# Optimization experiments

Measured on AMD Instinct MI355X. Metric: run time of the kernel, lower is better.

## Reference

```python
import jax, jax.numpy as jnp
import numpy as np

DIM = 512
WINDOW = 8
HEADS = 16
HEAD_DIM = DIM // HEADS
SIGMA = 0.39
B = 2048
N = WINDOW * WINDOW


def gaussian_kernel(window_size, sigma):
    """Row-normalised Gaussian attention mask K_sigma (M^2 x M^2)."""
    c = jnp.arange(window_size, dtype=jnp.float32)
    gy, gx = jnp.meshgrid(c, c, indexing='ij')
    pos = jnp.stack([gy.flatten(), gx.flatten()], -1)  # [M^2, 2]
    diff = pos[None, :, :] - pos[:, None, :]           # [M^2, M^2, 2]
    K = jnp.exp(-(diff ** 2).sum(-1) / (2.0 * sigma ** 2))
    return K / K.sum(-1, keepdims=True)


def setup_inputs() -> dict:
    key = jax.random.key(0)
    k1, k2, k3, k4, k5 = jax.random.split(key, 5)
    x = jax.random.normal(k1, (B, N, DIM), dtype=jnp.float32)
    # spectral_norm at inference is just a fixed scaling of the weight; we
    # model the (already-normalised) weights as plain dense params.
    w_qkv = jax.random.normal(k2, (DIM, 3 * DIM), dtype=jnp.float32) * (DIM ** -0.5)
    b_qkv = jax.random.normal(k3, (3 * DIM,), dtype=jnp.float32) * 0.02
    w_proj = jax.random.normal(k4, (DIM, DIM), dtype=jnp.float32) * (DIM ** -0.5)
    b_proj = jax.random.normal(k5, (DIM,), dtype=jnp.float32) * 0.02
    return {"x": x, "w_qkv": w_qkv, "b_qkv": b_qkv, "w_proj": w_proj, "b_proj": b_proj}


def reference(x, w_qkv, b_qkv, w_proj, b_proj):
    Bb, Nn, C = x.shape
    scale = HEAD_DIM ** -0.5
    qkv = (x @ w_qkv + b_qkv).reshape(Bb, Nn, 3, HEADS, HEAD_DIM)
    qkv = jnp.transpose(qkv, (2, 0, 3, 1, 4))  # [3, B, H, N, D]
    q, k, v = qkv[0], qkv[1], qkv[2]
    attn = jnp.einsum('bhnd,bhmd->bhnm', q, k) * scale  # [B, H, N, N]
    K_s = gaussian_kernel(WINDOW, SIGMA)                 # [N, N]
    attn = jax.nn.softmax(attn * K_s, axis=-1)
    out = jnp.einsum('bhnm,bhmd->bhnd', attn, v)         # [B, H, N, D]
    out = jnp.transpose(out, (0, 2, 1, 3)).reshape(Bb, Nn, C)
    return out @ w_proj + b_proj
```

## Files before the change

### kernel.cpp

```cpp
#include <hip/hip_runtime.h>
#include <hip/hip_bf16.h>
#include <stdint.h>

typedef __bf16 bf16;
typedef __bf16 bf16x8 __attribute__((ext_vector_type(8)));
typedef float f32x4 __attribute__((ext_vector_type(4)));
typedef unsigned short u16t;
typedef unsigned int u32t;

#define MFMA16(a, b, c) __builtin_amdgcn_mfma_f32_16x16x32_bf16((a), (b), (c), 0, 0, 0)

typedef const void __attribute__((address_space(1))) cg_void;
typedef void __attribute__((address_space(3))) lds_void;
#define GLL16(g, l) __builtin_amdgcn_global_load_lds((cg_void*)(g), (lds_void*)(l), 16, 0, 0)
#define VWAIT(n) asm volatile("s_waitcnt vmcnt(" #n ")" ::: "memory")

#define OFF_FLAG   0
#define OFF_BQKV   256
#define OFF_BPROJ  6400
#define OFF_WQKVT  8448
#define OFF_WPROJT 1581312
#define OFF_QKV    2105600
#define OFF_XB     404758784


__global__ __launch_bounds__(256) void k_detect(const u16t* x, u32t* flag) {
    __shared__ int cnt;
    if (threadIdx.x == 0) cnt = 0;
    __syncthreads();
    u16t h = x[threadIdx.x * 2];
    int e = (h >> 7) & 0xFF;
    int ok = (h == 0) || (e >= 100 && e <= 134);
    atomicAdd(&cnt, ok);
    __syncthreads();
    if (threadIdx.x == 0) flag[0] = (cnt >= 200) ? 1u : 0u;
}

__global__ __launch_bounds__(256) void k_cvt(const float* x, bf16* xb, const u32t* flagp) {
    if (flagp[0]) return;
    const size_t TOT = (size_t)131072 * 512;
    size_t i = (size_t)(blockIdx.x * 256 + threadIdx.x) * 8;
    const size_t stride = (size_t)gridDim.x * 256 * 8;
    for (; i < TOT; i += stride) {
        float4 v0 = *(const float4*)(x + i);
        float4 v1 = *(const float4*)(x + i + 4);
        bf16x8 h;
        h[0] = (bf16)v0.x; h[1] = (bf16)v0.y; h[2] = (bf16)v0.z; h[3] = (bf16)v0.w;
        h[4] = (bf16)v1.x; h[5] = (bf16)v1.y; h[6] = (bf16)v1.z; h[7] = (bf16)v1.w;
        *(bf16x8*)(xb + i) = h;
    }
}

template <int N, bool PERM>
__global__ __launch_bounds__(256) void k_trans(const void* W, bf16* Wt, const u32t* flagp) {
    __shared__ float T[64][65];
    const int isbf = (int)flagp[0];
    const int n0 = blockIdx.x * 64, k0 = blockIdx.y * 64;
    const int t = threadIdx.x;
    const int lc = t & 63, lr = t >> 6;
#pragma unroll
    for (int rr = 0; rr < 16; ++rr) {
        int row = rr * 4 + lr;
        int col = n0 + lc;
        int srcc = col;
        if (PERM) {
            int h = col / 96, r = col % 96;
            srcc = (r >> 5) * 512 + h * 32 + (r & 31);
        }
        size_t g = (size_t)(k0 + row) * N + srcc;
        float v = isbf ? (float)((const bf16*)W)[g] : ((const float*)W)[g];
        T[row][lc] = v;
    }
    __syncthreads();
#pragma unroll
    for (int rr = 0; rr < 16; ++rr) {
        int row = rr * 4 + lr;
        Wt[(size_t)(n0 + row) * 512 + k0 + lc] = (bf16)T[lc][row];
    }
}

__global__ __launch_bounds__(256) void k_bias(const void* b_qkv, const void* b_proj,
                                              const u32t* flagp, char* ws) {
    float* bq = (float*)(ws + OFF_BQKV);
    float* bp = (float*)(ws + OFF_BPROJ);
    const int isbf = (int)flagp[0];
    int gid = blockIdx.x * 256 + threadIdx.x;
    if (gid < 1536) {
        int h = gid / 96, r = gid % 96;
        int src = (r >> 5) * 512 + h * 32 + (r & 31);
        bq[gid] = isbf ? (float)((const bf16*)b_qkv)[src] : ((const float*)b_qkv)[src];
    } else if (gid < 2048) {
        int o = gid - 1536;
        bp[o] = isbf ? (float)((const bf16*)b_proj)[o] : ((const float*)b_proj)[o];
    }
}

template <int NTOT>
__global__ __launch_bounds__(512, 2) void k_gemm(const void* Ax, const bf16* Axb, const bf16* Bt,
                                                 const float* bias, void* Cp,
                                                 const u32t* flagp, int omode) {
    __shared__ __align__(16) u16t As[2 * 16384];
    __shared__ __align__(16) u16t Bs[2 * 16384];
    constexpr int NBN = NTOT / 256;
    const int isbf = (int)flagp[0];
    const int out_bf16 = (omode == 1) || isbf;
    const bf16* Ab = isbf ? (const bf16*)Ax : Axb;

    const int t = threadIdx.x;
    const int w = t >> 6, lane = t & 63;
    const int ln = lane & 15, qd = lane >> 4;
    const int wm = w >> 2, wn = w & 3;

    const int flat = blockIdx.x;
    const int xcd = flat & 7, slot = flat >> 3;
    const int n_idx = slot % NBN, grp = slot / NBN;
    const int m0 = (grp * 8 + xcd) * 256;
    const int n0 = n_idx * 256;

    const int l8 = lane >> 3, pc = lane & 7;
    const int cs8 = (pc ^ l8) * 8;
    u32t aoff[2][2], boff[2][2];
    int adst[2][2], bdst[2][2];
#pragma unroll
    for (int s = 0; s < 2; ++s)
#pragma unroll
        for (int q2 = 0; q2 < 2; ++q2) {
            int rA = q2 * 128 + s * 64 + w * 8;
            aoff[s][q2] = (u32t)(m0 + rA + l8) * 512 + cs8;
            adst[s][q2] = rA * 64;
            int rB = (q2 * 2 + (w >> 2)) * 64 + s * 32 + (w & 3) * 8;
            boff[s][q2] = (u32t)(n0 + rB + l8) * 512 + cs8;
            bdst[s][q2] = rB * 64;
        }

    const int p0 = (qd ^ (ln & 7)) * 8;
    int abase[4], bbase[2];
#pragma unroll
    for (int i = 0; i < 4; ++i) abase[i] = (wm * 128 + i * 16 + ln) * 64 + p0;
#pragma unroll
    for (int j = 0; j < 2; ++j) bbase[j] = (wn * 64 + j * 16 + ln) * 64 + p0;

    f32x4 acc[8][4];
    f32x4 zero = {0.f, 0.f, 0.f, 0.f};
#pragma unroll
    for (int i = 0; i < 8; ++i)
#pragma unroll
        for (int j = 0; j < 4; ++j) acc[i][j] = zero;

    auto stageA = [&](int s, int buf, int kt) {
#pragma unroll
        for (int q2 = 0; q2 < 2; ++q2)
            GLL16(Ab + aoff[s][q2] + kt * 64, &As[buf * 16384 + adst[s][q2]]);
    };
    auto stageB = [&](int s, int buf, int kt) {
#pragma unroll
        for (int q2 = 0; q2 < 2; ++q2)
            GLL16(Bt + boff[s][q2] + kt * 64, &Bs[buf * 16384 + bdst[s][q2]]);
    };

#define PH(BUF, QM, QN, STG, WAITOP)                                             \
    {                                                                            \
        bf16x8 af[4][2], bv[2][2];                                               \
        const u16t* Ap = &As[(BUF) * 16384 + (QM) * 4096];                       \
        const u16t* Bp = &Bs[(BUF) * 16384 + (QN) * 2048];                       \
        _Pragma("unroll") for (int i = 0; i < 4; ++i) {                          \
            af[i][0] = *(const bf16x8*)(const void*)&Ap[abase[i]];               \
            af[i][1] = *(const bf16x8*)(const void*)&Ap[abase[i] ^ 32];          \
        }                                                                        \
        _Pragma("unroll") for (int j = 0; j < 2; ++j) {                          \
            bv[j][0] = *(const bf16x8*)(const void*)&Bp[bbase[j]];               \
            bv[j][1] = *(const bf16x8*)(const void*)&Bp[bbase[j] ^ 32];          \
        }                                                                        \
        STG;                                                                     \
        WAITOP;                                                                  \
        __builtin_amdgcn_s_barrier();                                            \
        __builtin_amdgcn_s_setprio(1);                                           \
        _Pragma("unroll") for (int i = 0; i < 4; ++i)                            \
            _Pragma("unroll") for (int j = 0; j < 2; ++j) {                      \
                acc[(QM) * 4 + i][(QN) * 2 + j] =                                \
                    MFMA16(af[i][0], bv[j][0], acc[(QM) * 4 + i][(QN) * 2 + j]); \
                acc[(QM) * 4 + i][(QN) * 2 + j] =                                \
                    MFMA16(af[i][1], bv[j][1], acc[(QM) * 4 + i][(QN) * 2 + j]); \
            }                                                                    \
        __builtin_amdgcn_s_setprio(0);                                           \
        __builtin_amdgcn_s_barrier();                                            \
    }

    stageA(0, 0, 0);
    stageB(0, 0, 0);
    stageB(1, 0, 0);
    stageA(1, 0, 0);
    VWAIT(4);
    __builtin_amdgcn_s_barrier();

    for (int kt = 0; kt < 7; ++kt) {
        const int buf = kt & 1, nb = buf ^ 1, k1 = kt + 1;
        PH(buf, 0, 0, stageA(0, nb, k1), VWAIT(4));
        PH(buf, 0, 1, stageB(0, nb, k1), VWAIT(4));
        PH(buf, 1, 0, stageB(1, nb, k1), VWAIT(6));
        PH(buf, 1, 1, stageA(1, nb, k1), VWAIT(4));
    }
    PH(1, 0, 0, (void)0, VWAIT(2));
    PH(1, 0, 1, (void)0, VWAIT(0));
    PH(1, 1, 0, (void)0, (void)0);
    PH(1, 1, 1, (void)0, (void)0);
#undef PH

    float bj[4];
#pragma unroll
    for (int j = 0; j < 4; ++j) bj[j] = bias[n0 + wn * 64 + j * 16 + ln];

    if (out_bf16) {
        bf16* C = (bf16*)Cp;
#pragma unroll
        for (int i = 0; i < 8; ++i)
#pragma unroll
            for (int j = 0; j < 4; ++j)
#pragma unroll
                for (int rr = 0; rr < 4; ++rr) {
                    size_t row = (size_t)m0 + wm * 128 + i * 16 + qd * 4 + rr;
                    int col = n0 + wn * 64 + j * 16 + ln;
                    C[row * NTOT + col] = (bf16)(acc[i][j][rr] + bj[j]);
                }
    } else {
        float* C = (float*)Cp;
#pragma unroll
        for (int i = 0; i < 8; ++i)
#pragma unroll
            for (int j = 0; j < 4; ++j)
#pragma unroll
                for (int rr = 0; rr < 4; ++rr) {
                    size_t row = (size_t)m0 + wm * 128 + i * 16 + qd * 4 + rr;
                    int col = n0 + wn * 64 + j * 16 + ln;
                    C[row * NTOT + col] = acc[i][j][rr] + bj[j];
                }
    }
}

__global__ __launch_bounds__(256, 3) void k_fuse4(const void* Ax, const bf16* Axb,
                                                  const bf16* Bt, const float* bias,
                                                  bf16* attnout, const u32t* flagp) {
    __shared__ __align__(16) u16t pool[26624];
    const int isbf = (int)flagp[0];
    const bf16* Ab = isbf ? (const bf16*)Ax : Axb;

    const int t = threadIdx.x;
    const int w = t >> 6, lane = t & 63;
    const int ln = lane & 15, qd = lane >> 4, q8 = qd * 8;
    const int wm = w >> 1, wn = w & 1;

    const int flat = blockIdx.x;
    const int xcd = flat & 7, slot = flat >> 3;
    const int n_idx = slot & 7, mgrp = slot >> 3;
    const int blkm = mgrp * 8 + xcd;
    const int m0 = blkm * 128;
    const int n0 = n_idx * 192;
    const int win = blkm * 2 + wm;
    const int g = n_idx * 2 + wn;

    const int l4 = lane >> 2;
    const int csw = ((lane & 3) ^ (l4 & 3)) * 8;

    u32t asrc[2];
    int adst[2];
#pragma unroll
    for (int q = 0; q < 2; ++q) {
        int r0 = w * 32 + q * 16;
        asrc[q] = (u32t)(m0 + r0 + l4) * 512 + csw;
        adst[q] = r0 * 32;
    }
    u32t bsrc[3];
    int bdst[3];
#pragma unroll
    for (int r = 0; r < 3; ++r) {
        int rb = r * 32 + (w & 1) * 16 + (w >> 1) * 96;
        bsrc[r] = (u32t)(n0 + rb + l4) * 512 + csw;
        bdst[r] = rb * 32;
    }

    const int ck = (qd ^ (ln & 3)) * 8;
    int afo[4], bfo[6];
#pragma unroll
    for (int i = 0; i < 4; ++i) afo[i] = (wm * 64 + i * 16 + ln) * 32 + ck;
#pragma unroll
    for (int j = 0; j < 6; ++j) bfo[j] = (wn * 96 + j * 16 + ln) * 32 + ck;

    f32x4 acc[4][6];
    f32x4 zero = {0.f, 0.f, 0.f, 0.f};
#pragma unroll
    for (int i = 0; i < 4; ++i)
#pragma unroll
        for (int j = 0; j < 6; ++j) acc[i][j] = zero;

    auto ST_A = [&](int buf, int kt) {
#pragma unroll
        for (int q = 0; q < 2; ++q)
            GLL16(Ab + asrc[q] + kt * 32, &pool[buf * 4096 + adst[q]]);
    };
    auto ST_R = [&](int r, int buf, int kt) {
        GLL16(Bt + bsrc[r] + kt * 32, &pool[8192 + buf * 6144 + bdst[r]]);
    };

    ST_A(0, 0);
    ST_R(0, 0, 0);
    ST_R(1, 0, 0);
    ST_R(2, 0, 0);
    VWAIT(2);
    __builtin_amdgcn_s_barrier();

    for (int kt = 0; kt < 16; ++kt) {
        const int buf = kt & 1, nb = buf ^ 1;
        const u16t* Abuf = &pool[buf * 4096];
        const u16t* Bbuf = &pool[8192 + buf * 6144];
        bf16x8 af[4], bv[2];

#pragma unroll
        for (int i = 0; i < 4; ++i)
            af[i] = *(const bf16x8*)(const void*)&Abuf[afo[i]];
        bv[0] = *(const bf16x8*)(const void*)&Bbuf[bfo[0]];
        bv[1] = *(const bf16x8*)(const void*)&Bbuf[bfo[1]];
        if (kt < 15) { ST_A(nb, kt + 1); ST_R(0, nb, kt + 1); VWAIT(4); }
        else VWAIT(1);
        __builtin_amdgcn_s_barrier();
        __builtin_amdgcn_s_setprio(1);
#pragma unroll
        for (int i = 0; i < 4; ++i) {
            acc[i][0] = MFMA16(af[i], bv[0], acc[i][0]);
            acc[i][1] = MFMA16(af[i], bv[1], acc[i][1]);
        }
        __builtin_amdgcn_s_setprio(0);
        __builtin_amdgcn_s_barrier();

        bv[0] = *(const bf16x8*)(const void*)&Bbuf[bfo[2]];
        bv[1] = *(const bf16x8*)(const void*)&Bbuf[bfo[3]];
        if (kt < 15) { ST_R(1, nb, kt + 1); VWAIT(4); }
        else VWAIT(0);
        __builtin_amdgcn_s_barrier();
        __builtin_amdgcn_s_setprio(1);
#pragma unroll
        for (int i = 0; i < 4; ++i) {
            acc[i][2] = MFMA16(af[i], bv[0], acc[i][2]);
            acc[i][3] = MFMA16(af[i], bv[1], acc[i][3]);
        }
        __builtin_amdgcn_s_setprio(0);
        __builtin_amdgcn_s_barrier();

        bv[0] = *(const bf16x8*)(const void*)&Bbuf[bfo[4]];
        bv[1] = *(const bf16x8*)(const void*)&Bbuf[bfo[5]];
        if (kt < 15) { ST_R(2, nb, kt + 1); VWAIT(2); }
        __builtin_amdgcn_s_barrier();
        __builtin_amdgcn_s_setprio(1);
#pragma unroll
        for (int i = 0; i < 4; ++i) {
            acc[i][4] = MFMA16(af[i], bv[0], acc[i][4]);
            acc[i][5] = MFMA16(af[i], bv[1], acc[i][5]);
        }
        __builtin_amdgcn_s_setprio(0);
        __builtin_amdgcn_s_barrier();
    }

    float bj[6];
#pragma unroll
    for (int j = 0; j < 6; ++j) bj[j] = bias[g * 96 + j * 16 + ln];
    u16t* pw = &pool[w * 6656];
#pragma unroll
    for (int i = 0; i < 4; ++i)
#pragma unroll
        for (int j = 0; j < 6; ++j) {
            int part = j >> 1;
            int d = (j & 1) * 16 + ln;
#pragma unroll
            for (int rr = 0; rr < 4; ++rr) {
                int tok = i * 16 + qd * 4 + rr;
                bf16 val = (bf16)(acc[i][j][rr] + bj[j]);
                int idx;
                if (part == 2)
                    idx = 4608 + tok * 32 +
                          (((d >> 3) ^ (((tok >> 3) ^ tok) & 3)) << 3) + (d & 7);
                else
                    idx = part * 2048 + tok * 32 +
                          (((d >> 3) ^ ((tok >> 1) & 3)) << 3) + (d & 7);
                *(bf16*)&pw[idx] = val;
            }
        }

    {
        const int hcol = g * 32;
        const int qswz = (qd ^ ((ln >> 1) & 3)) * 8;

        bf16x8 aq[4], bk[4];
#pragma unroll
        for (int i = 0; i < 4; ++i)
            aq[i] = *(const bf16x8*)(const void*)&pw[(i * 16 + ln) * 32 + qswz];
#pragma unroll
        for (int j = 0; j < 4; ++j)
            bk[j] = *(const bf16x8*)(const void*)&pw[2048 + (j * 16 + ln) * 32 + qswz];

        f32x4 zro = {0.f, 0.f, 0.f, 0.f};
        f32x4 s[4][4];
#pragma unroll
        for (int i = 0; i < 4; ++i)
#pragma unroll
            for (int j = 0; j < 4; ++j) s[i][j] = MFMA16(aq[i], bk[j], zro);

        const float INV2S2 = 3.28731097961867f;
        {
            int c = lane & 7;
            float S1 = 0.f;
#pragma unroll
            for (int c2 = 0; c2 < 8; ++c2) {
                int dd = c - c2;
                S1 += __expf(-(float)(dd * dd) * INV2S2);
            }
            float invS1 = 1.0f / S1;
            const int ymb = ln >> 3, xm = ln & 7, yq = qd >> 1, xq = (qd & 1) * 4;
            float FY[4][4], FX[4];
#pragma unroll
            for (int i = 0; i < 4; ++i) {
                int yn = 2 * i + yq;
                float gg = __shfl(invS1, yn, 64);
#pragma unroll
                for (int j = 0; j < 4; ++j) {
                    int dy = yn - (2 * j + ymb);
                    FY[i][j] = __expf(-(float)(dy * dy) * INV2S2) * gg;
                }
            }
#pragma unroll
            for (int rr = 0; rr < 4; ++rr) {
                int xn = xq + rr;
                int dx = xn - xm;
                FX[rr] = __expf(-(float)(dx * dx) * INV2S2) * __shfl(invS1, xn, 64);
            }

            const float SCALE = 0.17677669529663687f;
#pragma unroll
            for (int i = 0; i < 4; ++i)
#pragma unroll
                for (int rr = 0; rr < 4; ++rr) {
                    float lj[4];
                    float mx = -1e30f;
#pragma unroll
                    for (int j = 0; j < 4; ++j) {
                        lj[j] = s[i][j][rr] * SCALE * FY[i][j] * FX[rr];
                        mx = fmaxf(mx, lj[j]);
                    }
                    mx = fmaxf(mx, __shfl_xor(mx, 1));
                    mx = fmaxf(mx, __shfl_xor(mx, 2));
                    mx = fmaxf(mx, __shfl_xor(mx, 4));
                    mx = fmaxf(mx, __shfl_xor(mx, 8));
                    float sum = 0.f;
#pragma unroll
                    for (int j = 0; j < 4; ++j) {
                        lj[j] = __expf(lj[j] - mx);
                        sum += lj[j];
                    }
                    sum += __shfl_xor(sum, 1);
                    sum += __shfl_xor(sum, 2);
                    sum += __shfl_xor(sum, 4);
                    sum += __shfl_xor(sum, 8);
                    float inv = 1.0f / sum;
                    int n = i * 16 + qd * 4 + rr;
#pragma unroll
                    for (int j = 0; j < 4; ++j) {
                        bf16 pv = (bf16)(lj[j] * inv);
                        *(bf16*)&pw[n * 72 + j * 16 + ln] = pv;
                    }
                }
        }

        f32x4 o[4][2];
#pragma unroll
        for (int i = 0; i < 4; ++i) {
            o[i][0] = zro;
            o[i][1] = zro;
        }
#pragma unroll
        for (int kc = 0; kc < 64; kc += 32) {
            bf16x8 bv2[2];
#pragma unroll
            for (int j2 = 0; j2 < 2; ++j2) {
                int cc = j2 * 2 + (ln >> 3);
#pragma unroll
                for (int jj = 0; jj < 8; ++jj) {
                    int rv = kc + q8 + jj;
                    bv2[j2][jj] = *(const bf16*)&pw[4608 + rv * 32 +
                                                   ((cc ^ (((rv >> 3) ^ rv) & 3)) << 3) + (ln & 7)];
                }
            }
#pragma unroll
            for (int i = 0; i < 4; ++i) {
                bf16x8 ap = *(const bf16x8*)(const void*)&pw[(i * 16 + ln) * 72 + kc + q8];
#pragma unroll
                for (int j2 = 0; j2 < 2; ++j2) o[i][j2] = MFMA16(ap, bv2[j2], o[i][j2]);
            }
        }
#pragma unroll
        for (int i = 0; i < 4; ++i)
#pragma unroll
            for (int j2 = 0; j2 < 2; ++j2)
#pragma unroll
                for (int rr = 0; rr < 4; ++rr)
                    attnout[((size_t)win * 64 + i * 16 + qd * 4 + rr) * 512 +
                            hcol + j2 * 16 + ln] = (bf16)(o[i][j2][rr]);
    }
}

extern "C" void kernel_launch(void* const* d_in, const int* in_sizes, int n_in,
                              void* d_out, int out_size, void* d_ws, size_t ws_size,
                              hipStream_t stream) {
    const void* x = d_in[0];
    const void* w_qkv = d_in[1];
    const void* b_qkv = d_in[2];
    const void* w_proj = d_in[3];
    const void* b_proj = d_in[4];
    char* ws = (char*)d_ws;
    u32t* flag = (u32t*)(ws + OFF_FLAG);
    bf16* wqkvT = (bf16*)(ws + OFF_WQKVT);
    bf16* wprojT = (bf16*)(ws + OFF_WPROJT);
    float* bq = (float*)(ws + OFF_BQKV);
    float* bp = (float*)(ws + OFF_BPROJ);
    bf16* attnout = (bf16*)(ws + OFF_QKV);
    bf16* xb = (bf16*)(ws + OFF_XB);

    k_detect<<<1, 256, 0, stream>>>((const u16t*)x, flag);
    k_cvt<<<2048, 256, 0, stream>>>((const float*)x, xb, flag);
    k_trans<1536, true><<<dim3(24, 8), 256, 0, stream>>>(w_qkv, wqkvT, flag);
    k_trans<512, false><<<dim3(8, 8), 256, 0, stream>>>(w_proj, wprojT, flag);
    k_bias<<<8, 256, 0, stream>>>(b_qkv, b_proj, flag, ws);
    k_fuse4<<<8192, 256, 0, stream>>>(x, xb, wqkvT, bq, attnout, flag);
    k_gemm<512><<<1024, 512, 0, stream>>>((const void*)attnout, attnout, wprojT, bp, d_out, flag, 2);
}
```

Measured before the change: 856.6 us.

## Repack LDS tiles as token pairs and halve k-step in projection GEMM

Both the QKV-fused kernel and the output projection GEMM now stage two rows (tokens) per 64-element LDS line with a new XOR swizzle, and fragment reads use a matching token-pair addressing. The projection GEMM drops from a 64-wide to a 32-wide k-tile with 16 iterations, halving its LDS footprint and loading A fragments only on alternating phases so they are reused across two N quadrants. The aim is fewer LDS bank conflicts, fewer LDS reads and possibly higher occupancy, at the price of more loop iterations and barriers per k.

```diff
diff --git a/kernel.cpp b/kernel.cpp
--- a/kernel.cpp
+++ b/kernel.cpp
@@ -22,6 +22,7 @@
 #define OFF_WPROJT 1581312
 #define OFF_QKV    2105600
 #define OFF_XB     404758784
+
 
 
 __global__ __launch_bounds__(256) void k_detect(const u16t* x, u32t* flag) {
@@ -99,8 +100,8 @@
 __global__ __launch_bounds__(512, 2) void k_gemm(const void* Ax, const bf16* Axb, const bf16* Bt,
                                                  const float* bias, void* Cp,
                                                  const u32t* flagp, int omode) {
-    __shared__ __align__(16) u16t As[2 * 16384];
-    __shared__ __align__(16) u16t Bs[2 * 16384];
+    __shared__ __align__(16) u16t As[2 * 8192];
+    __shared__ __align__(16) u16t Bs[2 * 8192];
     constexpr int NBN = NTOT / 256;
     const int isbf = (int)flagp[0];
     const int out_bf16 = (omode == 1) || isbf;
@@ -117,28 +118,29 @@
     const int m0 = (grp * 8 + xcd) * 256;
     const int n0 = n_idx * 256;
 
-    const int l8 = lane >> 3, pc = lane & 7;
-    const int cs8 = (pc ^ l8) * 8;
-    u32t aoff[2][2], boff[2][2];
-    int adst[2][2], bdst[2][2];
-#pragma unroll
-    for (int s = 0; s < 2; ++s)
-#pragma unroll
-        for (int q2 = 0; q2 < 2; ++q2) {
-            int rA = q2 * 128 + s * 64 + w * 8;
-            aoff[s][q2] = (u32t)(m0 + rA + l8) * 512 + cs8;
-            adst[s][q2] = rA * 64;
-            int rB = (q2 * 2 + (w >> 2)) * 64 + s * 32 + (w & 3) * 8;
-            boff[s][q2] = (u32t)(n0 + rB + l8) * 512 + cs8;
-            bdst[s][q2] = rB * 64;
-        }
-
-    const int p0 = (qd ^ (ln & 7)) * 8;
+    const int l8 = lane >> 3, p8 = lane & 7;
+    const int cl = p8 ^ l8;
+    const int tok_l = 2 * l8 + (cl >> 2);
+    const int koff = (cl & 3) * 8;
+
+    u32t asrc[2], bsrc[2];
+    int adst[2], bdst[2];
+#pragma unroll
+    for (int s = 0; s < 2; ++s) {
+        int RsA = s * 32 + (w >> 2) * 64 + (w & 3) * 8;
+        asrc[s] = (u32t)(m0 + 2 * RsA + tok_l) * 512 + koff;
+        adst[s] = RsA * 64;
+        int RsB = s * 16 + (w >> 1) * 32 + (w & 1) * 8;
+        bsrc[s] = (u32t)(n0 + 2 * RsB + tok_l) * 512 + koff;
+        bdst[s] = RsB * 64;
+    }
+
+    const int fph = (((ln & 1) * 4 + qd) ^ ((ln >> 1) & 7)) * 8;
     int abase[4], bbase[2];
 #pragma unroll
-    for (int i = 0; i < 4; ++i) abase[i] = (wm * 128 + i * 16 + ln) * 64 + p0;
-#pragma unroll
-    for (int j = 0; j < 2; ++j) bbase[j] = (wn * 64 + j * 16 + ln) * 64 + p0;
+    for (int i = 0; i < 4; ++i) abase[i] = (wm * 64 + i * 8 + (ln >> 1)) * 64 + fph;
+#pragma unroll
+    for (int j = 0; j < 2; ++j) bbase[j] = (wn * 32 + j * 8 + (ln >> 1)) * 64 + fph;
 
     f32x4 acc[8][4];
     f32x4 zero = {0.f, 0.f, 0.f, 0.f};
@@ -148,63 +150,57 @@
         for (int j = 0; j < 4; ++j) acc[i][j] = zero;
 
     auto stageA = [&](int s, int buf, int kt) {
-#pragma unroll
-        for (int q2 = 0; q2 < 2; ++q2)
-            GLL16(Ab + aoff[s][q2] + kt * 64, &As[buf * 16384 + adst[s][q2]]);
+        GLL16(Ab + asrc[s] + kt * 32, &As[buf * 8192 + adst[s]]);
     };
     auto stageB = [&](int s, int buf, int kt) {
-#pragma unroll
-        for (int q2 = 0; q2 < 2; ++q2)
-            GLL16(Bt + boff[s][q2] + kt * 64, &Bs[buf * 16384 + bdst[s][q2]]);
+        GLL16(Bt + bsrc[s] + kt * 32, &Bs[buf * 8192 + bdst[s]]);
     };
 
-#define PH(BUF, QM, QN, STG, WAITOP)                                             \
-    {                                                                            \
-        bf16x8 af[4][2], bv[2][2];                                               \
-        const u16t* Ap = &As[(BUF) * 16384 + (QM) * 4096];                       \
-        const u16t* Bp = &Bs[(BUF) * 16384 + (QN) * 2048];                       \
-        _Pragma("unroll") for (int i = 0; i < 4; ++i) {                          \
-            af[i][0] = *(const bf16x8*)(const void*)&Ap[abase[i]];               \
-            af[i][1] = *(const bf16x8*)(const void*)&Ap[abase[i] ^ 32];          \
-        }                                                                        \
-        _Pragma("unroll") for (int j = 0; j < 2; ++j) {                          \
-            bv[j][0] = *(const bf16x8*)(const void*)&Bp[bbase[j]];               \
-            bv[j][1] = *(const bf16x8*)(const void*)&Bp[bbase[j] ^ 32];          \
-        }                                                                        \
-        STG;                                                                     \
-        WAITOP;                                                                  \
-        __builtin_amdgcn_s_barrier();                                            \
-        __builtin_amdgcn_s_setprio(1);                                           \
-        _Pragma("unroll") for (int i = 0; i < 4; ++i)                            \
-            _Pragma("unroll") for (int j = 0; j < 2; ++j) {                      \
-                acc[(QM) * 4 + i][(QN) * 2 + j] =                                \
-                    MFMA16(af[i][0], bv[j][0], acc[(QM) * 4 + i][(QN) * 2 + j]); \
-                acc[(QM) * 4 + i][(QN) * 2 + j] =                                \
-                    MFMA16(af[i][1], bv[j][1], acc[(QM) * 4 + i][(QN) * 2 + j]); \
-            }                                                                    \
-        __builtin_amdgcn_s_setprio(0);                                           \
-        __builtin_amdgcn_s_barrier();                                            \
+#define PHX(BUF, QM, QN, LOADA, STG, WAITOP)                                    \
+    {                                                                           \
+        if (LOADA) {                                                            \
+            _Pragma("unroll") for (int i = 0; i < 4; ++i)                       \
+                af[i] = *(const bf16x8*)(const void*)                           \
+                    &As[(BUF) * 8192 + (QM) * 2048 + abase[i]];                 \
+        }                                                                       \
+        _Pragma("unroll") for (int j = 0; j < 2; ++j)                           \
+            bv[j] = *(const bf16x8*)(const void*)                               \
+                &Bs[(BUF) * 8192 + (QN) * 1024 + bbase[j]];                     \
+        STG;                                                                    \
+        WAITOP;                                                                 \
+        __builtin_amdgcn_s_barrier();                                           \
+        __builtin_amdgcn_s_setprio(1);                                          \
+        _Pragma("unroll") for (int i = 0; i < 4; ++i)                           \
+            _Pragma("unroll") for (int j = 0; j < 2; ++j)                       \
+                acc[(QM) * 4 + i][(QN) * 2 + j] =                               \
+                    MFMA16(af[i], bv[j], acc[(QM) * 4 + i][(QN) * 2 + j]);      \
+        __builtin_amdgcn_s_setprio(0);                                          \
+        __builtin_amdgcn_s_barrier();                                           \
     }
 
     stageA(0, 0, 0);
     stageB(0, 0, 0);
     stageB(1, 0, 0);
     stageA(1, 0, 0);
-    VWAIT(4);
+    VWAIT(2);
     __builtin_amdgcn_s_barrier();
 
-    for (int kt = 0; kt < 7; ++kt) {
+    for (int kt = 0; kt < 16; ++kt) {
         const int buf = kt & 1, nb = buf ^ 1, k1 = kt + 1;
-        PH(buf, 0, 0, stageA(0, nb, k1), VWAIT(4));
-        PH(buf, 0, 1, stageB(0, nb, k1), VWAIT(4));
-        PH(buf, 1, 0, stageB(1, nb, k1), VWAIT(6));
-        PH(buf, 1, 1, stageA(1, nb, k1), VWAIT(4));
-    }
-    PH(1, 0, 0, (void)0, VWAIT(2));
-    PH(1, 0, 1, (void)0, VWAIT(0));
-    PH(1, 1, 0, (void)0, (void)0);
-    PH(1, 1, 1, (void)0, (void)0);
-#undef PH
+        bf16x8 af[4], bv[2];
+        if (kt < 15) {
+            PHX(buf, 0, 0, 1, stageA(0, nb, k1), VWAIT(2));
+            PHX(buf, 0, 1, 0, stageB(0, nb, k1), VWAIT(2));
+            PHX(buf, 1, 0, 1, stageB(1, nb, k1), (void)0);
+            PHX(buf, 1, 1, 0, stageA(1, nb, k1), VWAIT(2));
+        } else {
+            PHX(buf, 0, 0, 1, (void)0, VWAIT(1));
+            PHX(buf, 0, 1, 0, (void)0, VWAIT(0));
+            PHX(buf, 1, 0, 1, (void)0, (void)0);
+            PHX(buf, 1, 1, 0, (void)0, (void)0);
+        }
+    }
+#undef PHX
 
     float bj[4];
 #pragma unroll
@@ -237,7 +233,7 @@
     }
 }
 
-__global__ __launch_bounds__(256, 3) void k_fuse4(const void* Ax, const bf16* Axb,
+__global__ __launch_bounds__(256, 3) void k_fuse5(const void* Ax, const bf16* Axb,
                                                   const bf16* Bt, const float* bias,
                                                   bf16* attnout, const u32t* flagp) {
     __shared__ __align__(16) u16t pool[26624];
@@ -258,32 +254,34 @@
     const int win = blkm * 2 + wm;
     const int g = n_idx * 2 + wn;
 
-    const int l4 = lane >> 2;
-    const int csw = ((lane & 3) ^ (l4 & 3)) * 8;
+    const int l8 = lane >> 3, p8 = lane & 7;
+    const int cl = p8 ^ l8;
+    const int tok_l = 2 * l8 + (cl >> 2);
+    const int koff = (cl & 3) * 8;
 
     u32t asrc[2];
     int adst[2];
 #pragma unroll
     for (int q = 0; q < 2; ++q) {
-        int r0 = w * 32 + q * 16;
-        asrc[q] = (u32t)(m0 + r0 + l4) * 512 + csw;
-        adst[q] = r0 * 32;
+        int Rs = w * 16 + q * 8;
+        asrc[q] = (u32t)(m0 + 2 * Rs + tok_l) * 512 + koff;
+        adst[q] = Rs * 64;
     }
     u32t bsrc[3];
     int bdst[3];
 #pragma unroll
     for (int r = 0; r < 3; ++r) {
-        int rb = r * 32 + (w & 1) * 16 + (w >> 1) * 96;
-        bsrc[r] = (u32t)(n0 + rb + l4) * 512 + csw;
-        bdst[r] = rb * 32;
-    }
-
-    const int ck = (qd ^ (ln & 3)) * 8;
+        int Rs = (w & 1) * 48 + r * 16 + (w >> 1) * 8;
+        bsrc[r] = (u32t)(n0 + 2 * Rs + tok_l) * 512 + koff;
+        bdst[r] = Rs * 64;
+    }
+
+    const int fph = (((ln & 1) * 4 + qd) ^ ((ln >> 1) & 7)) * 8;
     int afo[4], bfo[6];
 #pragma unroll
-    for (int i = 0; i < 4; ++i) afo[i] = (wm * 64 + i * 16 + ln) * 32 + ck;
-#pragma unroll
-    for (int j = 0; j < 6; ++j) bfo[j] = (wn * 96 + j * 16 + ln) * 32 + ck;
+    for (int i = 0; i < 4; ++i) afo[i] = (wm * 32 + i * 8 + (ln >> 1)) * 64 + fph;
+#pragma unroll
+    for (int j = 0; j < 6; ++j) bfo[j] = (wn * 48 + j * 8 + (ln >> 1)) * 64 + fph;
 
     f32x4 acc[4][6];
     f32x4 zero = {0.f, 0.f, 0.f, 0.f};
@@ -527,6 +525,6 @@
     k_trans<1536, true><<<dim3(24, 8), 256, 0, stream>>>(w_qkv, wqkvT, flag);
     k_trans<512, false><<<dim3(8, 8), 256, 0, stream>>>(w_proj, wprojT, flag);
     k_bias<<<8, 256, 0, stream>>>(b_qkv, b_proj, flag, ws);
-    k_fuse4<<<8192, 256, 0, stream>>>(x, xb, wqkvT, bq, attnout, flag);
+    k_fuse5<<<8192, 256, 0, stream>>>(x, xb, wqkvT, bq, attnout, flag);
     k_gemm<512><<<1024, 512, 0, stream>>>((const void*)attnout, attnout, wprojT, bp, d_out, flag, 2);
 }
```

Measured after the change: 864.2 us. Within noise of the previous version (+0.9%).
